# Kernel tuning notes

Hardware: AMD Instinct MI355X
Metric: run time of the kernel (lower is better)

## Reference

```python
import jax, jax.numpy as jnp
import numpy as np
from jax import lax

C = 128
B, H, W = 8, 128, 128
HW = H * W


def _layernorm(x, w, b):
    # x: [b,c,h,w]; WithBias LN over channel dim c (matches to_3d -> LN(last dim=c) -> to_4d)
    mu = jnp.mean(x, axis=1, keepdims=True)
    var = jnp.mean((x - mu) ** 2, axis=1, keepdims=True)
    xn = (x - mu) / jnp.sqrt(var + 1e-5)
    return xn * w[None, :, None, None] + b[None, :, None, None]


def _conv1x1(x, w, b):
    # x: [b,c,h,w], w: [out,in]
    return jnp.einsum('bchw,oc->bohw', x, w) + b[None, :, None, None]


def _dwconv3(x, w, b):
    # depthwise 3x3, w: [c,1,3,3]
    c = x.shape[1]
    y = lax.conv_general_dilated(x, w, window_strides=(1, 1),
                                 padding=((1, 1), (1, 1)),
                                 feature_group_count=c,
                                 dimension_numbers=('NCHW', 'OIHW', 'NCHW'))
    return y + b[None, :, None, None]


def _l2norm(x):
    # torch F.normalize(dim=-1): x / max(||x||, 1e-12)
    n = jnp.sqrt(jnp.sum(x * x, axis=-1, keepdims=True))
    return x / jnp.maximum(n, 1e-12)


def setup_inputs() -> dict:
    key = jax.random.key(0)
    ks = jax.random.split(key, 12)
    s = 0.02
    return {
        'pre': jax.random.normal(ks[0], (B, HW, C), jnp.float32),
        'cur': jax.random.normal(ks[1], (B, HW, C), jnp.float32),
        'ln1_w': jnp.ones((C,), jnp.float32),
        'ln1_b': jnp.zeros((C,), jnp.float32),
        'ln2_w': jnp.ones((C,), jnp.float32),
        'ln2_b': jnp.zeros((C,), jnp.float32),
        'q_w1': jax.random.normal(ks[2], (C, C), jnp.float32) * s,
        'q_b1': jnp.zeros((C,), jnp.float32),
        'q_w2': jax.random.normal(ks[3], (C, 1, 3, 3), jnp.float32) * s,
        'q_b2': jnp.zeros((C,), jnp.float32),
        'kv_w1': jax.random.normal(ks[4], (2 * C, C), jnp.float32) * s,
        'kv_b1': jnp.zeros((2 * C,), jnp.float32),
        'kv_w2': jax.random.normal(ks[5], (2 * C, 1, 3, 3), jnp.float32) * s,
        'kv_b2': jnp.zeros((2 * C,), jnp.float32),
        'out_w': jax.random.normal(ks[6], (C, C), jnp.float32) * s,
        'out_b': jnp.zeros((C,), jnp.float32),
    }


def reference(pre, cur, ln1_w, ln1_b, ln2_w, ln2_b,
              q_w1, q_b1, q_w2, q_b2,
              kv_w1, kv_b1, kv_w2, kv_b2,
              out_w, out_b):
    b, hw, c = cur.shape
    h = w = int(np.sqrt(hw))
    # [b,hw,c] -> [b,c,h,w]
    cur4 = jnp.transpose(cur.reshape(b, h, w, c), (0, 3, 1, 2))
    pre4 = jnp.transpose(pre.reshape(b, h, w, c), (0, 3, 1, 2))

    pre_ln = _layernorm(pre4, ln1_w, ln1_b)
    cur_ln = _layernorm(cur4, ln2_w, ln2_b)

    q = _dwconv3(_conv1x1(cur_ln, q_w1, q_b1), q_w2, q_b2)        # [b,c,h,w]
    kv = _dwconv3(_conv1x1(pre_ln, kv_w1, kv_b1), kv_w2, kv_b2)   # [b,2c,h,w]
    k, v = jnp.split(kv, 2, axis=1)

    q = _l2norm(q.reshape(b, c, hw))
    k = _l2norm(k.reshape(b, c, hw))
    v = v.reshape(b, c, hw)

    att = jax.nn.softmax(jnp.einsum('bcn,bdn->bcd', q, k), axis=-1)  # [b,c,c]
    out = jnp.einsum('bcd,bdn->bcn', att, v).reshape(b, c, h, w)

    out = _conv1x1(out, out_w, out_b) + cur4                         # residual
    # [b,c,h,w] -> [b,hw,c]
    return jnp.transpose(out.reshape(b, c, hw), (0, 2, 1))
```

## Files before the change

kernel.cpp:

```cpp
#include <hip/hip_runtime.h>

typedef __attribute__((ext_vector_type(4))) float f32x4;
typedef __attribute__((ext_vector_type(2))) float f32x2;
typedef __attribute__((ext_vector_type(8))) short s16x8;
typedef __attribute__((ext_vector_type(4))) short s16x4;
typedef __bf16 bf16x8 __attribute__((ext_vector_type(8)));

__device__ __forceinline__ short f2bf(float f) {
  union { float f; unsigned u; } c; c.f = f;
  unsigned r = c.u + 0x7fffu + ((c.u >> 16) & 1u);
  return (short)(r >> 16);
}
__device__ __forceinline__ float bf2f(short s) {
  union { unsigned u; float f; } c; c.u = ((unsigned)(unsigned short)s) << 16;
  return c.f;
}

__global__ void k0_prep(const float* __restrict__ qw1, const float* __restrict__ qb1,
                        const float* __restrict__ kvw1, const float* __restrict__ kvb1,
                        const float* __restrict__ ln1w, const float* __restrict__ ln1b,
                        const float* __restrict__ ln2w, const float* __restrict__ ln2b,
                        short* __restrict__ Wq, short* __restrict__ Wk, short* __restrict__ Wv,
                        float* __restrict__ T)
{
  const int path = blockIdx.x;
  const int o = threadIdx.x >> 1, hf = threadIdx.x & 1;
  const float *W, *bias, *lw, *lb; short* Wo; float *t1, *t2;
  if (path == 0)      { W = qw1;            bias = qb1;       lw = ln2w; lb = ln2b; Wo = Wq; t1 = T;       t2 = T + 128; }
  else if (path == 1) { W = kvw1;           bias = kvb1;      lw = ln1w; lb = ln1b; Wo = Wk; t1 = T + 256; t2 = T + 384; }
  else                { W = kvw1 + 16384;   bias = kvb1+128;  lw = ln1w; lb = ln1b; Wo = Wv; t1 = T + 512; t2 = T + 640; }
  float s1 = 0.f, s2 = 0.f;
  for (int g = 0; g < 64; g++) {
    const int c = hf * 64 + g;
    const float w = W[o * 128 + c];
    const float wp = w * lw[c];
    s1 += wp; s2 += w * lb[c];
    Wo[o * 128 + c] = f2bf(wp);
  }
  s1 += __shfl_xor(s1, 1);
  s2 += __shfl_xor(s2, 1);
  if (hf == 0) { t1[o] = s1; t2[o] = s2 + bias[o]; }
}

__device__ __forceinline__ void k1_stage(const float* __restrict__ X, int mblk,
                                         short (&At)[128][136], f32x2 (&rowstat)[128],
                                         int tid)
{
  const int r = tid >> 1, hf = tid & 1;
  const float* src = X + ((size_t)(mblk * 128 + r)) * 128 + hf * 64;
  float s1 = 0.f, s2 = 0.f;
#pragma unroll
  for (int g = 0; g < 8; g++) {
    const f32x4 v0 = *(const f32x4*)(src + g * 8);
    const f32x4 v1 = *(const f32x4*)(src + g * 8 + 4);
    s16x8 o;
#pragma unroll
    for (int j = 0; j < 4; j++) {
      s1 += v0[j] + v1[j]; s2 += v0[j] * v0[j] + v1[j] * v1[j];
      o[j] = f2bf(v0[j]); o[4 + j] = f2bf(v1[j]);
    }
    *(s16x8*)&At[r][hf * 64 + g * 8] = o;
  }
  s1 += __shfl_xor(s1, 1);
  s2 += __shfl_xor(s2, 1);
  if (hf == 0) {
    const float mu = s1 * (1.f / 128.f);
    const float var = s2 * (1.f / 128.f) - mu * mu;
    rowstat[r] = (f32x2){mu, rsqrtf(var + 1e-5f)};
  }
}

__device__ __forceinline__ void k1_gemm_epi(const short (&At)[128][136],
                                            const f32x2 (&rowstat)[128],
                                            const short* __restrict__ Wp,
                                            const float* __restrict__ t1,
                                            const float* __restrict__ t2,
                                            short* __restrict__ Yout,
                                            int b, int pl0,
                                            int wv, int l16, int quad, int kof)
{
  f32x4 acc[2][8];
#pragma unroll
  for (int i = 0; i < 2; i++)
#pragma unroll
    for (int j = 0; j < 8; j++) acc[i][j] = (f32x4){0.f, 0.f, 0.f, 0.f};

#pragma unroll
  for (int ks = 0; ks < 4; ks++) {
    const int kb = ks * 32 + kof;
    const bf16x8 a0 = *(const bf16x8*)&At[wv * 32 + l16][kb];
    const bf16x8 a1 = *(const bf16x8*)&At[wv * 32 + 16 + l16][kb];
#pragma unroll
    for (int j = 0; j < 8; j++) {
      const bf16x8 bv = *(const bf16x8*)(Wp + (j * 16 + l16) * 128 + kb);
      acc[0][j] = __builtin_amdgcn_mfma_f32_16x16x32_bf16(a0, bv, acc[0][j], 0, 0, 0);
      acc[1][j] = __builtin_amdgcn_mfma_f32_16x16x32_bf16(a1, bv, acc[1][j], 0, 0, 0);
    }
  }
  float t1v[8], t2v[8];
#pragma unroll
  for (int j = 0; j < 8; j++) { const int o = j * 16 + l16; t1v[j] = t1[o]; t2v[j] = t2[o]; }
#pragma unroll
  for (int i = 0; i < 2; i++) {
    const int pr = wv * 32 + i * 16 + quad * 4;
    f32x2 st[4];
#pragma unroll
    for (int rg = 0; rg < 4; rg++) st[rg] = rowstat[pr + rg];
#pragma unroll
    for (int j = 0; j < 8; j++) {
      const int o = j * 16 + l16;
      s16x4 pk;
#pragma unroll
      for (int rg = 0; rg < 4; rg++) {
        const float y = st[rg].y * acc[i][j][rg] - st[rg].x * st[rg].y * t1v[j] + t2v[j];
        pk[rg] = f2bf(y);
      }
      *(s16x4*)(Yout + ((size_t)(b * 128 + o)) * 16384 + pl0 + pr) = pk;
    }
  }
}

__global__ __launch_bounds__(256, 4)
void k1_ln_gemm(const float* __restrict__ cur, const float* __restrict__ pre,
                const short* __restrict__ Wq, const short* __restrict__ Wk,
                const short* __restrict__ Wv, const float* __restrict__ T,
                short* __restrict__ Yq, short* __restrict__ Yk, short* __restrict__ Yv)
{
  __shared__ __attribute__((aligned(16))) short At[128][136];
  __shared__ f32x2 rowstat[128];
  const int tid = threadIdx.x, mblk = blockIdx.x;
  const int b = mblk >> 7;
  const int pl0 = (mblk & 127) * 128;
  const int wv = tid >> 6, lane = tid & 63, l16 = lane & 15, quad = lane >> 4, kof = quad * 8;

  k1_stage(cur, mblk, At, rowstat, tid);
  __syncthreads();
  k1_gemm_epi(At, rowstat, Wq, T, T + 128, Yq, b, pl0, wv, l16, quad, kof);
  __syncthreads();

  k1_stage(pre, mblk, At, rowstat, tid);
  __syncthreads();
  k1_gemm_epi(At, rowstat, Wk, T + 256, T + 384, Yk, b, pl0, wv, l16, quad, kof);
  k1_gemm_epi(At, rowstat, Wv, T + 512, T + 640, Yv, b, pl0, wv, l16, quad, kof);
}

__global__ __launch_bounds__(256, 4)
void k2_plane(const short* __restrict__ Yq, const short* __restrict__ Yk,
              const short* __restrict__ Yv,
              const float* __restrict__ qw2, const float* __restrict__ qb2,
              const float* __restrict__ kvw2, const float* __restrict__ kvb2,
              short* __restrict__ qo, short* __restrict__ ko, short* __restrict__ vo,
              float* __restrict__ nq, float* __restrict__ nk)
{
  __shared__ __attribute__((aligned(16))) short tile[130][144];
  __shared__ float red[256];
  const int tid = threadIdx.x, bx = blockIdx.x;
  const int path = bx >> 10, rem = bx & 1023;
  const int b = rem >> 7, c = rem & 127;
  const short* in; const float* w2p; float bsv; short* outp; float* np;
  if (path == 0)      { in = Yq; w2p = qw2 + c * 9;          bsv = qb2[c];        outp = qo; np = nq; }
  else if (path == 1) { in = Yk; w2p = kvw2 + c * 9;         bsv = kvb2[c];       outp = ko; np = nk; }
  else                { in = Yv; w2p = kvw2 + (128 + c) * 9; bsv = kvb2[128 + c]; outp = vo; np = nullptr; }

  const short* plane = in + ((size_t)(b * 128 + c)) * 16384;
#pragma unroll
  for (int g = 0; g < 8; g++) {
    const int e = (g * 256 + tid) * 8;
    *(s16x8*)&tile[(e >> 7) + 1][(e & 127) + 8] = *(const s16x8*)(plane + e);
  }
  const s16x8 z8 = (s16x8){0, 0, 0, 0, 0, 0, 0, 0};
  if (tid < 128) *(s16x8*)&tile[tid + 1][136] = z8;
  if (tid < 36) { const int rr = (tid / 18) * 129, cc = (tid % 18) * 8; *(s16x8*)&tile[rr][cc] = z8; }
  __syncthreads();

  float wt[9];
#pragma unroll
  for (int j = 0; j < 9; j++) wt[j] = w2p[j];
  const int rr = tid >> 1, hfc = tid & 1;

  float A0[8], A1[8], A2[8];
  {
    const int ca = 8 + hfc * 64;
    const s16x8 a0 = *(const s16x8*)&tile[rr][ca];
    const s16x8 a1 = *(const s16x8*)&tile[rr + 1][ca];
    const s16x8 a2 = *(const s16x8*)&tile[rr + 2][ca];
#pragma unroll
    for (int x = 0; x < 8; x++) { A0[x] = bf2f(a0[x]); A1[x] = bf2f(a1[x]); A2[x] = bf2f(a2[x]); }
  }
  float p0, p1, p2;
  if (hfc) { p0 = bf2f(tile[rr][71]); p1 = bf2f(tile[rr + 1][71]); p2 = bf2f(tile[rr + 2][71]); }
  else { p0 = p1 = p2 = 0.f; }

  float ss = 0.f;
  short* oplane = outp + ((size_t)(b * 128 + c)) * 16384 + rr * 128 + hfc * 64;
#pragma unroll
  for (int g = 0; g < 8; g++) {
    const int cb = 16 + hfc * 64 + g * 8;
    const s16x8 b0 = *(const s16x8*)&tile[rr][cb];
    const s16x8 b1 = *(const s16x8*)&tile[rr + 1][cb];
    const s16x8 b2 = *(const s16x8*)&tile[rr + 2][cb];
    float B0[8], B1[8], B2[8];
#pragma unroll
    for (int x = 0; x < 8; x++) { B0[x] = bf2f(b0[x]); B1[x] = bf2f(b1[x]); B2[x] = bf2f(b2[x]); }
    s16x8 ov;
#pragma unroll
    for (int x = 0; x < 8; x++) {
      const float l0 = x ? A0[x - 1] : p0, l1 = x ? A1[x - 1] : p1, l2 = x ? A2[x - 1] : p2;
      const float r0 = (x < 7) ? A0[x + 1] : B0[0];
      const float r1 = (x < 7) ? A1[x + 1] : B1[0];
      const float r2 = (x < 7) ? A2[x + 1] : B2[0];
      float s = bsv;
      s += wt[0] * l0 + wt[1] * A0[x] + wt[2] * r0;
      s += wt[3] * l1 + wt[4] * A1[x] + wt[5] * r1;
      s += wt[6] * l2 + wt[7] * A2[x] + wt[8] * r2;
      ov[x] = f2bf(s); ss += s * s;
    }
    *(s16x8*)(oplane + g * 8) = ov;
    p0 = A0[7]; p1 = A1[7]; p2 = A2[7];
#pragma unroll
    for (int x = 0; x < 8; x++) { A0[x] = B0[x]; A1[x] = B1[x]; A2[x] = B2[x]; }
  }
  red[tid] = ss;
  __syncthreads();
  if (tid < 64) {
    float t = red[tid] + red[tid + 64] + red[tid + 128] + red[tid + 192];
#pragma unroll
    for (int m = 32; m >= 1; m >>= 1) t += __shfl_xor(t, m);
    if (tid == 0 && np) np[b * 128 + c] = t;
  }
}

__global__ __launch_bounds__(256, 2)
void k3_gram(const short* __restrict__ qo, const short* __restrict__ ko,
             float* __restrict__ Gp)
{
  const int tid = threadIdx.x, bx = blockIdx.x;
  const int b = bx >> 6, sp = bx & 63;
  const int wv = tid >> 6, lane = tid & 63, l16 = lane & 15, quad = lane >> 4, kof = quad * 8;
  f32x4 acc[2][8];
#pragma unroll
  for (int i = 0; i < 2; i++)
#pragma unroll
    for (int j = 0; j < 8; j++) acc[i][j] = (f32x4){0.f, 0.f, 0.f, 0.f};

  const short* qb = qo + (size_t)b * 128 * 16384 + sp * 256 + kof;
  const short* kb = ko + (size_t)b * 128 * 16384 + sp * 256 + kof;
#pragma unroll
  for (int ks = 0; ks < 8; ks++) {
    const int n0 = ks * 32;
    const bf16x8 a0 = *(const bf16x8*)(qb + (size_t)(wv * 32 + l16) * 16384 + n0);
    const bf16x8 a1 = *(const bf16x8*)(qb + (size_t)(wv * 32 + 16 + l16) * 16384 + n0);
#pragma unroll
    for (int j = 0; j < 8; j++) {
      const bf16x8 bv = *(const bf16x8*)(kb + (size_t)(j * 16 + l16) * 16384 + n0);
      acc[0][j] = __builtin_amdgcn_mfma_f32_16x16x32_bf16(a0, bv, acc[0][j], 0, 0, 0);
      acc[1][j] = __builtin_amdgcn_mfma_f32_16x16x32_bf16(a1, bv, acc[1][j], 0, 0, 0);
    }
  }
  float* gp = Gp + ((size_t)(sp * 8 + b)) * 16384;
#pragma unroll
  for (int i = 0; i < 2; i++)
#pragma unroll
    for (int j = 0; j < 8; j++)
#pragma unroll
      for (int rg = 0; rg < 4; rg++)
        gp[(wv * 32 + i * 16 + quad * 4 + rg) * 128 + j * 16 + l16] = acc[i][j][rg];
}

__global__ void k4a_softmax(const float* __restrict__ Gp,
                            const float* __restrict__ nq, const float* __restrict__ nk,
                            float* __restrict__ att)
{
  const int tid = threadIdx.x;
  const int b = blockIdx.x >> 4, cb = (blockIdx.x & 15) * 8;
  const int r = tid >> 5, dsi = tid & 31;
  const int c = cb + r, d0 = dsi * 4;
  f32x4 a = (f32x4){0.f, 0.f, 0.f, 0.f};
  for (int ks = 0; ks < 64; ks++)
    a += *(const f32x4*)(Gp + ((size_t)(ks * 8 + b)) * 16384 + c * 128 + d0);
  const float qn = fmaxf(sqrtf(nq[b * 128 + c]), 1e-12f);
  f32x4 sc;
#pragma unroll
  for (int j = 0; j < 4; j++) {
    const float kn = fmaxf(sqrtf(nk[b * 128 + d0 + j]), 1e-12f);
    sc[j] = a[j] / (qn * kn);
  }
  float mx = fmaxf(fmaxf(sc[0], sc[1]), fmaxf(sc[2], sc[3]));
#pragma unroll
  for (int m = 16; m >= 1; m >>= 1) mx = fmaxf(mx, __shfl_xor(mx, m));
  f32x4 e; float sum = 0.f;
#pragma unroll
  for (int j = 0; j < 4; j++) { e[j] = __expf(sc[j] - mx); sum += e[j]; }
#pragma unroll
  for (int m = 16; m >= 1; m >>= 1) sum += __shfl_xor(sum, m);
  const float inv = 1.f / sum;
  f32x4 o;
#pragma unroll
  for (int j = 0; j < 4; j++) o[j] = e[j] * inv;
  *(f32x4*)(att + (size_t)b * 16384 + c * 128 + d0) = o;
}

__global__ void k4b_mw(const float* __restrict__ att, const float* __restrict__ outw,
                       short* __restrict__ Mb)
{
  __shared__ float at[128][8];
  const int tid = threadIdx.x, bx = blockIdx.x;
  const int b = bx >> 4, d0 = (bx & 15) * 8;
  {
    const int cc = tid >> 1, q = tid & 1;
    *(f32x4*)&at[cc][q * 4] = *(const f32x4*)(att + (size_t)b * 16384 + cc * 128 + d0 + q * 4);
  }
  __syncthreads();
  const int o = tid & 127, dq = (tid >> 7) * 4;
  f32x4 acc = (f32x4){0.f, 0.f, 0.f, 0.f};
  const float* wr = outw + o * 128;
  for (int cc = 0; cc < 128; cc++) {
    const float w = wr[cc];
    const f32x4 a = *(const f32x4*)&at[cc][dq];
    acc += w * a;
  }
  s16x4 pk;
#pragma unroll
  for (int rg = 0; rg < 4; rg++) pk[rg] = f2bf(acc[rg]);
  *(s16x4*)(Mb + ((size_t)(b * 128 + o)) * 128 + d0 + dq) = pk;
}

__global__ __launch_bounds__(256, 3)
void k5_out(const short* __restrict__ Mb, const short* __restrict__ vp,
            const float* __restrict__ outb, const float* __restrict__ cur,
            float* __restrict__ out)
{
  __shared__ __attribute__((aligned(16))) short Vt[128][136];
  const int tid = threadIdx.x;
  const int b = blockIdx.x >> 7, nb = (blockIdx.x & 127) * 128;
  {
    const int d = tid >> 1, hf = tid & 1;
    const short* src = vp + ((size_t)(b * 128 + d)) * 16384 + nb + hf * 64;
#pragma unroll
    for (int g = 0; g < 8; g++) {
      const s16x8 v = *(const s16x8*)(src + g * 8);
#pragma unroll
      for (int x = 0; x < 8; x++) Vt[hf * 64 + g * 8 + x][d] = v[x];
    }
  }
  __syncthreads();
  const int wv = tid >> 6, lane = tid & 63, l16 = lane & 15, quad = lane >> 4, kof = quad * 8;
  f32x4 acc[2][8];
#pragma unroll
  for (int i = 0; i < 2; i++)
#pragma unroll
    for (int j = 0; j < 8; j++) acc[i][j] = (f32x4){0.f, 0.f, 0.f, 0.f};

  const short* m0 = Mb + ((size_t)(b * 128 + wv * 32 + l16)) * 128;
  const short* m1 = m0 + 16 * 128;
#pragma unroll
  for (int ks = 0; ks < 4; ks++) {
    const int kb = ks * 32 + kof;
    const bf16x8 a0 = *(const bf16x8*)(m0 + kb);
    const bf16x8 a1 = *(const bf16x8*)(m1 + kb);
#pragma unroll
    for (int j = 0; j < 8; j++) {
      const bf16x8 bv = *(const bf16x8*)&Vt[j * 16 + l16][kb];
      acc[0][j] = __builtin_amdgcn_mfma_f32_16x16x32_bf16(a0, bv, acc[0][j], 0, 0, 0);
      acc[1][j] = __builtin_amdgcn_mfma_f32_16x16x32_bf16(a1, bv, acc[1][j], 0, 0, 0);
    }
  }
#pragma unroll
  for (int i = 0; i < 2; i++) {
    const int o0 = wv * 32 + i * 16 + quad * 4;
    const f32x4 bias = *(const f32x4*)(outb + o0);
#pragma unroll
    for (int j = 0; j < 8; j++) {
      const int pos = nb + j * 16 + l16;
      const size_t idx = ((size_t)(b * 16384 + pos)) * 128 + o0;
      const f32x4 cv = *(const f32x4*)(cur + idx);
      f32x4 rr;
#pragma unroll
      for (int rg = 0; rg < 4; rg++) rr[rg] = acc[i][j][rg] + bias[rg] + cv[rg];
      *(f32x4*)(out + idx) = rr;
    }
  }
}

extern "C" void kernel_launch(void* const* d_in, const int* in_sizes, int n_in,
                              void* d_out, int out_size, void* d_ws, size_t ws_size,
                              hipStream_t stream) {
  const float* pre  = (const float*)d_in[0];
  const float* cur  = (const float*)d_in[1];
  const float* ln1w = (const float*)d_in[2];
  const float* ln1b = (const float*)d_in[3];
  const float* ln2w = (const float*)d_in[4];
  const float* ln2b = (const float*)d_in[5];
  const float* qw1  = (const float*)d_in[6];
  const float* qb1  = (const float*)d_in[7];
  const float* qw2  = (const float*)d_in[8];
  const float* qb2  = (const float*)d_in[9];
  const float* kvw1 = (const float*)d_in[10];
  const float* kvb1 = (const float*)d_in[11];
  const float* kvw2 = (const float*)d_in[12];
  const float* kvb2 = (const float*)d_in[13];
  const float* outw = (const float*)d_in[14];
  const float* outb = (const float*)d_in[15];

  char* ws = (char*)d_ws;
  short* Yq  = (short*)(ws);
  short* Yk  = (short*)(ws + 33554432);
  short* Yv  = (short*)(ws + 67108864);
  short* qo  = (short*)(ws + 100663296);
  short* ko  = (short*)(ws + 134217728);
  short* vo  = (short*)(ws + 167772160);
  float* Gp  = (float*)(ws);
  float* att = (float*)(ws + 33554432);
  short* Mb  = (short*)(ws + 34078720);
  char*  sm  = ws + 201326592;
  short* Wq  = (short*)(sm);
  short* Wk  = (short*)(sm + 32768);
  short* Wv  = (short*)(sm + 65536);
  float* T   = (float*)(sm + 98304);
  float* nq  = (float*)(sm + 102400);
  float* nk  = (float*)(sm + 106496);

  hipLaunchKernelGGL(k0_prep, dim3(3), dim3(256), 0, stream,
                     qw1, qb1, kvw1, kvb1, ln1w, ln1b, ln2w, ln2b, Wq, Wk, Wv, T);
  hipLaunchKernelGGL(k1_ln_gemm, dim3(1024), dim3(256), 0, stream,
                     cur, pre, Wq, Wk, Wv, T, Yq, Yk, Yv);
  hipLaunchKernelGGL(k2_plane, dim3(3072), dim3(256), 0, stream,
                     Yq, Yk, Yv, qw2, qb2, kvw2, kvb2, qo, ko, vo, nq, nk);
  hipLaunchKernelGGL(k3_gram, dim3(512), dim3(256), 0, stream, qo, ko, Gp);
  hipLaunchKernelGGL(k4a_softmax, dim3(128), dim3(256), 0, stream, Gp, nq, nk, att);
  hipLaunchKernelGGL(k4b_mw, dim3(128), dim3(256), 0, stream, att, outw, Mb);
  hipLaunchKernelGGL(k5_out, dim3(1024), dim3(256), 0, stream, Mb, vo, outb, cur, (float*)d_out);
}
```

Baseline: 438.2 us.

## Split LN-GEMM blocks per path with register prefetch and widen softmax grid

The fused LN+1x1 GEMM kernel now gives each block one projection path (q, k or v) and two 128-pixel tiles. The next tile is prefetched into registers while the current tile's GEMM runs, so global loads overlap MFMA work. This gives 1536 blocks instead of 1024, but the pre input is now loaded and normalized twice (once for k, once for v). Launch bounds drop to 3 blocks per CU to leave room for the prefetch registers. The softmax kernel is remapped so one wavefront handles a full row, giving twice as many blocks to spread the Gp partial-sum reduction.

```diff
diff --git a/kernel.cpp b/kernel.cpp
--- a/kernel.cpp
+++ b/kernel.cpp
@@ -42,17 +42,24 @@
   if (hf == 0) { t1[o] = s1; t2[o] = s2 + bias[o]; }
 }
 
-__device__ __forceinline__ void k1_stage(const float* __restrict__ X, int mblk,
-                                         short (&At)[128][136], f32x2 (&rowstat)[128],
-                                         int tid)
+__device__ __forceinline__ void k1_loadR(const float* __restrict__ src, f32x4 (&PR)[16])
+{
+#pragma unroll
+  for (int g = 0; g < 8; g++) {
+    PR[2 * g]     = *(const f32x4*)(src + g * 8);
+    PR[2 * g + 1] = *(const f32x4*)(src + g * 8 + 4);
+  }
+}
+
+__device__ __forceinline__ void k1_stageW(const f32x4 (&PR)[16], int tid,
+                                          short (&At)[128][136], f32x2 (&rowstat)[128])
 {
   const int r = tid >> 1, hf = tid & 1;
-  const float* src = X + ((size_t)(mblk * 128 + r)) * 128 + hf * 64;
   float s1 = 0.f, s2 = 0.f;
 #pragma unroll
   for (int g = 0; g < 8; g++) {
-    const f32x4 v0 = *(const f32x4*)(src + g * 8);
-    const f32x4 v1 = *(const f32x4*)(src + g * 8 + 4);
+    const f32x4 v0 = PR[2 * g];
+    const f32x4 v1 = PR[2 * g + 1];
     s16x8 o;
 #pragma unroll
     for (int j = 0; j < 4; j++) {
@@ -120,7 +127,7 @@
   }
 }
 
-__global__ __launch_bounds__(256, 4)
+__global__ __launch_bounds__(256, 3)
 void k1_ln_gemm(const float* __restrict__ cur, const float* __restrict__ pre,
                 const short* __restrict__ Wq, const short* __restrict__ Wk,
                 const short* __restrict__ Wv, const float* __restrict__ T,
@@ -128,20 +135,30 @@
 {
   __shared__ __attribute__((aligned(16))) short At[128][136];
   __shared__ f32x2 rowstat[128];
-  const int tid = threadIdx.x, mblk = blockIdx.x;
-  const int b = mblk >> 7;
-  const int pl0 = (mblk & 127) * 128;
+  const int tid = threadIdx.x, bx = blockIdx.x;
+  const int path = bx >> 9;
+  const int m0 = (bx & 511) * 2;
+  const float* X = (path == 0) ? cur : pre;
+  const short* Wp = (path == 0) ? Wq : (path == 1) ? Wk : Wv;
+  short* Yout = (path == 0) ? Yq : (path == 1) ? Yk : Yv;
+  const float* t1 = T + path * 256;
+  const float* t2 = t1 + 128;
   const int wv = tid >> 6, lane = tid & 63, l16 = lane & 15, quad = lane >> 4, kof = quad * 8;
-
-  k1_stage(cur, mblk, At, rowstat, tid);
-  __syncthreads();
-  k1_gemm_epi(At, rowstat, Wq, T, T + 128, Yq, b, pl0, wv, l16, quad, kof);
-  __syncthreads();
-
-  k1_stage(pre, mblk, At, rowstat, tid);
-  __syncthreads();
-  k1_gemm_epi(At, rowstat, Wk, T + 256, T + 384, Yk, b, pl0, wv, l16, quad, kof);
-  k1_gemm_epi(At, rowstat, Wv, T + 512, T + 640, Yv, b, pl0, wv, l16, quad, kof);
+  const int r = tid >> 1, hf = tid & 1;
+  const float* src0 = X + ((size_t)(m0 * 128 + r)) * 128 + hf * 64;
+
+  f32x4 PR[16];
+  k1_loadR(src0, PR);
+  k1_stageW(PR, tid, At, rowstat);
+  __syncthreads();
+  k1_loadR(src0 + 16384, PR);
+  k1_gemm_epi(At, rowstat, Wp, t1, t2, Yout, m0 >> 7, (m0 & 127) * 128,
+              wv, l16, quad, kof);
+  __syncthreads();
+  k1_stageW(PR, tid, At, rowstat);
+  __syncthreads();
+  k1_gemm_epi(At, rowstat, Wp, t1, t2, Yout, (m0 + 1) >> 7, ((m0 + 1) & 127) * 128,
+              wv, l16, quad, kof);
 }
 
 __global__ __launch_bounds__(256, 4)
@@ -272,32 +289,29 @@
                             float* __restrict__ att)
 {
   const int tid = threadIdx.x;
-  const int b = blockIdx.x >> 4, cb = (blockIdx.x & 15) * 8;
-  const int r = tid >> 5, dsi = tid & 31;
-  const int c = cb + r, d0 = dsi * 4;
-  f32x4 a = (f32x4){0.f, 0.f, 0.f, 0.f};
+  const int b = blockIdx.x >> 5;
+  const int c = (blockIdx.x & 31) * 4 + (tid >> 6);
+  const int lane = tid & 63;
+  const int d0 = lane * 2;
+  f32x2 a = (f32x2){0.f, 0.f};
   for (int ks = 0; ks < 64; ks++)
-    a += *(const f32x4*)(Gp + ((size_t)(ks * 8 + b)) * 16384 + c * 128 + d0);
+    a += *(const f32x2*)(Gp + ((size_t)(ks * 8 + b)) * 16384 + c * 128 + d0);
   const float qn = fmaxf(sqrtf(nq[b * 128 + c]), 1e-12f);
-  f32x4 sc;
-#pragma unroll
-  for (int j = 0; j < 4; j++) {
-    const float kn = fmaxf(sqrtf(nk[b * 128 + d0 + j]), 1e-12f);
-    sc[j] = a[j] / (qn * kn);
-  }
-  float mx = fmaxf(fmaxf(sc[0], sc[1]), fmaxf(sc[2], sc[3]));
-#pragma unroll
-  for (int m = 16; m >= 1; m >>= 1) mx = fmaxf(mx, __shfl_xor(mx, m));
-  f32x4 e; float sum = 0.f;
-#pragma unroll
-  for (int j = 0; j < 4; j++) { e[j] = __expf(sc[j] - mx); sum += e[j]; }
-#pragma unroll
-  for (int m = 16; m >= 1; m >>= 1) sum += __shfl_xor(sum, m);
+  const f32x2 nk2 = *(const f32x2*)(nk + b * 128 + d0);
+  f32x2 sc;
+  sc[0] = a[0] / (qn * fmaxf(sqrtf(nk2[0]), 1e-12f));
+  sc[1] = a[1] / (qn * fmaxf(sqrtf(nk2[1]), 1e-12f));
+  float mx = fmaxf(sc[0], sc[1]);
+#pragma unroll
+  for (int m = 32; m >= 1; m >>= 1) mx = fmaxf(mx, __shfl_xor(mx, m));
+  f32x2 e; float sum;
+  e[0] = __expf(sc[0] - mx); e[1] = __expf(sc[1] - mx);
+  sum = e[0] + e[1];
+#pragma unroll
+  for (int m = 32; m >= 1; m >>= 1) sum += __shfl_xor(sum, m);
   const float inv = 1.f / sum;
-  f32x4 o;
-#pragma unroll
-  for (int j = 0; j < 4; j++) o[j] = e[j] * inv;
-  *(f32x4*)(att + (size_t)b * 16384 + c * 128 + d0) = o;
+  f32x2 o; o[0] = e[0] * inv; o[1] = e[1] * inv;
+  *(f32x2*)(att + (size_t)b * 16384 + c * 128 + d0) = o;
 }
 
 __global__ void k4b_mw(const float* __restrict__ att, const float* __restrict__ outw,
@@ -422,12 +436,12 @@
 
   hipLaunchKernelGGL(k0_prep, dim3(3), dim3(256), 0, stream,
                      qw1, qb1, kvw1, kvb1, ln1w, ln1b, ln2w, ln2b, Wq, Wk, Wv, T);
-  hipLaunchKernelGGL(k1_ln_gemm, dim3(1024), dim3(256), 0, stream,
+  hipLaunchKernelGGL(k1_ln_gemm, dim3(1536), dim3(256), 0, stream,
                      cur, pre, Wq, Wk, Wv, T, Yq, Yk, Yv);
   hipLaunchKernelGGL(k2_plane, dim3(3072), dim3(256), 0, stream,
                      Yq, Yk, Yv, qw2, qb2, kvw2, kvb2, qo, ko, vo, nq, nk);
   hipLaunchKernelGGL(k3_gram, dim3(512), dim3(256), 0, stream, qo, ko, Gp);
-  hipLaunchKernelGGL(k4a_softmax, dim3(128), dim3(256), 0, stream, Gp, nq, nk, att);
+  hipLaunchKernelGGL(k4a_softmax, dim3(256), dim3(256), 0, stream, Gp, nq, nk, att);
   hipLaunchKernelGGL(k4b_mw, dim3(128), dim3(256), 0, stream, att, outw, Mb);
   hipLaunchKernelGGL(k5_out, dim3(1024), dim3(256), 0, stream, Mb, vo, outb, cur, (float*)d_out);
 }
```

Measured after the change: 426.3 us. 2.7% less time.
